# Performance work log

Measured on AMD Instinct MI355X. Metric: run time of the kernel, lower is better.

Reference implementation:

```python
import jax, jax.numpy as jnp
import numpy as np

N, H = 16, 200
EMB, H1, H2 = 64, 128, 64
NUM_SKILLS = 2000
D_USER, D_ITEM, D_LANG = 100, 100, 10
TIME_BINS = np.array([1, 3600, 24 * 3600, 7 * 24 * 3600], dtype=np.float32)
NUM_TIME_CATS = TIME_BINS.size + 2  # 6

# strictly-lower-triangular pair indices, row-major: pair (i, j) with j < i
PAIR_I, PAIR_J = np.tril_indices(H, k=-1)          # skill_indices, history_indices_selected
P = PAIR_I.size                                    # adjusted_history_len = H*(H-1)/2
ar = np.arange(H)
SUM_IDX = np.concatenate([ar * (ar - 1) // 2, [H * (H - 1) // 2]]).astype(np.int64)  # len H+1


def setup_inputs() -> dict:
    key = jax.random.key(0)
    ks = jax.random.split(key, 16)
    users = jax.random.normal(ks[0], (N, D_USER), jnp.float32)
    items = jax.random.normal(ks[1], (N * H, D_ITEM), jnp.float32)
    langs = jax.random.normal(ks[2], (N * H, D_LANG), jnp.float32)
    skills = jax.random.randint(ks[3], (N, H), 0, NUM_SKILLS)
    timestamps = jnp.sort(jax.random.uniform(ks[4], (N, H), jnp.float32) * 2e6, axis=1)
    targets = (jax.random.uniform(ks[5], (N, H)) > 0.5).astype(jnp.float32)
    mask = jnp.ones((N * H,), dtype=bool)
    emb_table = jax.random.normal(ks[6], (NUM_SKILLS, EMB), jnp.float32) * 0.1
    emb_table = emb_table.at[0].set(0.0)  # padding_idx=0
    W1 = jax.random.normal(ks[7], (H1, 2 * EMB + NUM_TIME_CATS), jnp.float32) * 0.05
    b1 = jnp.zeros((H1,), jnp.float32)
    W2 = jax.random.normal(ks[8], (H2, H1), jnp.float32) * 0.05
    b2 = jnp.zeros((H2,), jnp.float32)
    W3 = jax.random.normal(ks[9], (1, H2), jnp.float32) * 0.05
    b3 = jnp.zeros((1,), jnp.float32)
    num_features = D_USER + D_ITEM + D_LANG + NUM_SKILLS
    linW = jax.random.normal(ks[10], (1, num_features + 2 * NUM_SKILLS), jnp.float32) * 0.01
    linb = jnp.zeros((1,), jnp.float32)
    return {"users": users, "items": items, "langs": langs, "skills": skills,
            "timestamps": timestamps, "targets": targets, "mask": mask,
            "emb_table": emb_table, "W1": W1, "b1": b1, "W2": W2, "b2": b2,
            "W3": W3, "b3": b3, "linW": linW, "linb": linb}


def _forward(users, items, langs, skills, timestamps, targets, mask,
             emb_table, W1, b1, W2, b2, W3, b3, linW, linb):
    bins = jnp.asarray(TIME_BINS)
    pi = jnp.asarray(PAIR_I)
    pj = jnp.asarray(PAIR_J)
    # gather pair embeddings: [N*P, EMB]
    emb = emb_table[skills]                       # [N, H, EMB]
    e_i = emb[:, pi].reshape(-1, EMB)             # skill at position i
    e_j = emb[:, pj].reshape(-1, EMB)             # history skill j < i
    # time-delta categories
    dt = (timestamps[:, pi] - timestamps[:, pj]).reshape(-1)
    cats = jnp.sum(dt[:, None] > bins[None, :], axis=1) + 1
    pad = skills == 0
    pad_pair = pad[:, pi].reshape(-1) | pad[:, pj].reshape(-1)
    cats = jnp.where(pad_pair, 0, cats)
    dt_oh = jax.nn.one_hot(cats, NUM_TIME_CATS, dtype=jnp.float32)
    # pairwise similarity MLP -> tanh scalar, [N, P]
    x = jnp.concatenate([e_i, e_j, dt_oh], axis=1)
    h = jax.nn.relu(x @ W1.T + b1)
    h = jax.nn.relu(h @ W2.T + b2)
    sim = jnp.tanh(h @ W3.T + b3).reshape(N, P)

    sum_idx = jnp.asarray(SUM_IDX)

    def seg_sum(v):  # cumsum-based segment sum over pairs grouped by i -> [N, H]
        cs = jnp.concatenate([jnp.zeros((N, 1), v.dtype), jnp.cumsum(v, axis=1)], axis=1)
        return cs[:, sum_idx[1:]] - cs[:, sum_idx[:-1]]

    flat_skills = skills.reshape(-1)              # [N*H]
    padf = (flat_skills != 0).astype(jnp.float32)
    rows = jnp.arange(N * H)
    v_total = seg_sum(sim).reshape(-1) * padf
    v_correct = seg_sum(sim * targets[:, pi]).reshape(-1) * padf
    tcf = jnp.zeros((N * H, 2 * NUM_SKILLS), jnp.float32)
    tcf = tcf.at[rows, flat_skills].set(v_total)
    tcf = tcf.at[rows, flat_skills + NUM_SKILLS].set(v_correct)

    feats = jnp.concatenate([
        jnp.repeat(users, H, axis=0), items, langs,
        jax.nn.one_hot(flat_skills, NUM_SKILLS, dtype=jnp.float32), tcf], axis=1)
    logits = feats @ linW.T + linb                # [N*H, 1]
    preds = logits.reshape(-1)
    labels = targets.reshape(-1)
    maskf = mask.astype(jnp.float32)
    # BCEWithLogits (reduction='none') + z-term, z_weight=0.0; mask applied as weight
    bce = jnp.logaddexp(0.0, preds) - preds * labels
    eps = 1e-6
    yc = jnp.clip(labels, eps, 1.0 - eps)
    z = jnp.log(yc / (1.0 - yc))
    z_weight = 0.0
    loss = (bce + z_weight * jnp.square(z - preds)) * maskf
    return loss, jax.nn.sigmoid(preds), labels


def reference(users, items, langs, skills, timestamps, targets, mask,
              emb_table, W1, b1, W2, b2, W3, b3, linW, linb):
    return _forward(users, items, langs, skills, timestamps, targets, mask,
                    emb_table, W1, b1, W2, b2, W3, b3, linW, linb)
```

## Files before the change

### kernel.cpp

```cpp
#include <hip/hip_runtime.h>
#include <math.h>

#define N_B     16
#define H_LEN   200
#define NH      3200
#define EMB     64
#define HID1    128
#define HID2    64
#define NCAT    6
#define W1_COLS 134

#define TI 16
#define NTILE_I 13
#define NTRI (NTILE_I * (NTILE_I + 1) / 2)

#define WS_VT   0
#define WS_W2F  3200
#define WS_W1F  7296
#define WS_CF   15488

typedef __attribute__((ext_vector_type(8))) __bf16 bf16x8;
typedef __attribute__((ext_vector_type(8))) unsigned short ushort8;
typedef __attribute__((ext_vector_type(4))) float f32x4;

__device__ __forceinline__ unsigned short bfbits(float x) {
    return __builtin_bit_cast(unsigned short, (__bf16)x);
}

__global__ void k0_setup(const float* __restrict__ W1,
                         const float* __restrict__ b1,
                         const float* __restrict__ W2,
                         float* __restrict__ ws) {
    int idx = blockIdx.x * 256 + threadIdx.x;
    if (idx < 16384) {
        int e = idx & 7, l = (idx >> 3) & 63, ks = (idx >> 9) & 1;
        int nt = (idx >> 10) & 7, h = idx >> 13;
        int col = l & 15, quad = l >> 4;
        int c = nt * 16 + col;
        int kg = h * EMB + ks * 32 + quad * 8 + e;
        ((unsigned short*)(ws + WS_W1F))[idx] = bfbits(W1[c * W1_COLS + kg]);
        return;
    }
    idx -= 16384;
    if (idx < 8192) {
        int e = idx & 7, lane = (idx >> 3) & 63, f = idx >> 9;
        int mt = f >> 2, kk = f & 3, col = lane & 15, quad = lane >> 4;
        float w = W2[(mt * 16 + col) * HID1 + (kk * 4 + quad) * 8 + e];
        ((unsigned short*)(ws + WS_W2F))[idx] = bfbits(w);
        return;
    }
    idx -= 8192;
    if (idx < NCAT * HID1) {
        int c = idx >> 7, t = idx & 127;
        ws[WS_CF + idx] = W1[t * W1_COLS + 2 * EMB + c] + b1[t];
        return;
    }
    idx -= NCAT * HID1;
    if (idx < NH) ws[WS_VT + idx] = 0.f;
}

__global__ __launch_bounds__(256, 2)
void k2_mfma(const int* __restrict__ skills,
             const float* __restrict__ ts,
             const float* __restrict__ emb,
             const float* __restrict__ b2,
             const float* __restrict__ W3,
             const float* __restrict__ b3,
             float* __restrict__ ws) {
    __shared__ float esmI[TI][68];
    __shared__ float esmJ[TI][68];
    __shared__ float Asm[TI][132];
    __shared__ float Bsm[TI][132];
    __shared__ float Csm[NCAT][132];
    __shared__ float tsi[TI], tsj[TI];
    __shared__ int   ski[TI], skj[TI];

    int t = threadIdx.x, lane = t & 63, w = t >> 6;
    int col = lane & 15, quad = lane >> 4;

    int bid = blockIdx.x;
    int n = bid & 15;
    int tt = bid >> 4;
    int ti = (int)((sqrtf(8.f * (float)tt + 1.f) - 1.f) * 0.5f);
    while (ti * (ti + 1) / 2 > tt) --ti;
    while ((ti + 1) * (ti + 2) / 2 <= tt) ++ti;
    int tj = tt - ti * (ti + 1) / 2;
    int i0 = ti * TI, j0 = tj * TI;
    int base = n * H_LEN;
    bool diag = (ti == tj);

    {
        int r = t >> 4, c4 = t & 15;
        int gi = min(i0 + r, H_LEN - 1);
        int gj = min(j0 + r, H_LEN - 1);
        int si = skills[base + gi], sj2 = skills[base + gj];
        *(f32x4*)&esmI[r][c4 * 4] = *(const f32x4*)(emb + (size_t)si * EMB + c4 * 4);
        *(f32x4*)&esmJ[r][c4 * 4] = *(const f32x4*)(emb + (size_t)sj2 * EMB + c4 * 4);
        if (t < NCAT * 32) {
            int cr = t >> 5, cc = t & 31;
            *(f32x4*)&Csm[cr][cc * 4] = *(const f32x4*)(ws + WS_CF + cr * HID1 + cc * 4);
        }
        if (t < TI) {
            int gii = min(i0 + t, H_LEN - 1);
            int gjj = min(j0 + t, H_LEN - 1);
            tsi[t] = ts[base + gii]; ski[t] = skills[base + gii];
            tsj[t] = ts[base + gjj]; skj[t] = skills[base + gjj];
        }
    }
    __syncthreads();

    {
        int half = w >> 1;
        int ntb = (w & 1) * 4;
        const ushort8* w1f = (const ushort8*)(ws + WS_W1F) + half * 1024;
        float (*es)[68] = half ? esmJ : esmI;
        float (*zs)[132] = half ? Bsm : Asm;
        f32x4 acc[4] = {{0,0,0,0},{0,0,0,0},{0,0,0,0},{0,0,0,0}};
        #pragma unroll
        for (int ks = 0; ks < 2; ++ks) {
            f32x4 a0 = *(const f32x4*)&es[col][ks * 32 + quad * 8];
            f32x4 a1 = *(const f32x4*)&es[col][ks * 32 + quad * 8 + 4];
            bf16x8 af;
            #pragma unroll
            for (int e = 0; e < 4; ++e) { af[e] = (__bf16)a0[e]; af[4 + e] = (__bf16)a1[e]; }
            #pragma unroll
            for (int ntl = 0; ntl < 4; ++ntl) {
                bf16x8 bf = __builtin_bit_cast(bf16x8,
                    w1f[((ntb + ntl) * 2 + ks) * 64 + lane]);
                acc[ntl] = __builtin_amdgcn_mfma_f32_16x16x32_bf16(af, bf, acc[ntl], 0, 0, 0);
            }
        }
        #pragma unroll
        for (int ntl = 0; ntl < 4; ++ntl)
            #pragma unroll
            for (int r = 0; r < 4; ++r)
                zs[quad * 4 + r][(ntb + ntl) * 16 + col] = acc[ntl][r];
    }

    const ushort8* w2f = (const ushort8*)(ws + WS_W2F);
    bf16x8 afr[4][4];
    #pragma unroll
    for (int mt = 0; mt < 4; ++mt)
        #pragma unroll
        for (int kk = 0; kk < 4; ++kk)
            afr[mt][kk] = __builtin_bit_cast(bf16x8, w2f[(mt * 4 + kk) * 64 + lane]);
    f32x4 b2acc[4], w3f[4];
    #pragma unroll
    for (int mt = 0; mt < 4; ++mt)
        #pragma unroll
        for (int r = 0; r < 4; ++r) {
            int u = mt * 16 + quad * 4 + r;
            b2acc[mt][r] = b2[u];
            w3f[mt][r]   = W3[u];
        }
    float b3s = b3[0];
    __syncthreads();

    f32x4 braw[8];
    #pragma unroll
    for (int kk = 0; kk < 4; ++kk) {
        braw[2 * kk]     = *(const f32x4*)&Bsm[col][kk * 32 + quad * 8];
        braw[2 * kk + 1] = *(const f32x4*)&Bsm[col][kk * 32 + quad * 8 + 4];
    }
    int sj = skj[col]; float tsjv = tsj[col];

    #pragma unroll
    for (int s = 0; s < 4; ++s) {
        int ii = w * 4 + s;
        int gi = i0 + ii;
        if (gi >= H_LEN) continue;
        if (diag && ii == 0) continue;

        int si = ski[ii];  float tsiv = tsi[ii];
        float dtv = tsiv - tsjv;
        int cat = (si == 0 || sj == 0) ? 0
                : 1 + (dtv > 1.f) + (dtv > 3600.f) + (dtv > 86400.f) + (dtv > 604800.f);

        f32x4 acc[4];
        #pragma unroll
        for (int kk = 0; kk < 4; ++kk) {
            f32x4 a0 = *(const f32x4*)&Asm[ii][kk * 32 + quad * 8];
            f32x4 a1 = *(const f32x4*)&Asm[ii][kk * 32 + quad * 8 + 4];
            f32x4 c0 = *(const f32x4*)&Csm[cat][kk * 32 + quad * 8];
            f32x4 c1 = *(const f32x4*)&Csm[cat][kk * 32 + quad * 8 + 4];
            f32x4 t0 = a0 + braw[2 * kk] + c0;
            f32x4 t1 = a1 + braw[2 * kk + 1] + c1;
            t0 = __builtin_elementwise_max(t0, (f32x4)0.f);
            t1 = __builtin_elementwise_max(t1, (f32x4)0.f);
            bf16x8 v;
            #pragma unroll
            for (int e = 0; e < 4; ++e) { v[e] = (__bf16)t0[e]; v[4 + e] = (__bf16)t1[e]; }
            #pragma unroll
            for (int mt = 0; mt < 4; ++mt)
                acc[mt] = __builtin_amdgcn_mfma_f32_16x16x32_bf16(
                    afr[mt][kk], v, kk == 0 ? b2acc[mt] : acc[mt], 0, 0, 0);
        }

        f32x4 ps = {0.f, 0.f, 0.f, 0.f};
        #pragma unroll
        for (int mt = 0; mt < 4; ++mt) {
            f32x4 hp = __builtin_elementwise_max(acc[mt], (f32x4)0.f);
            ps = hp * w3f[mt] + ps;
        }
        float partial = (ps[0] + ps[1]) + (ps[2] + ps[3]);
        partial += __shfl_xor(partial, 16);
        partial += __shfl_xor(partial, 32);
        float xc = fminf(fmaxf(partial + b3s, -15.f), 15.f);
        float e2 = __expf(2.f * xc);
        float sim = (e2 - 1.f) / (e2 + 1.f);

        int gj = j0 + col;
        bool valid = (gj < gi);
        sim = valid ? sim : 0.f;
        sim += __shfl_xor(sim, 1);
        sim += __shfl_xor(sim, 2);
        sim += __shfl_xor(sim, 4);
        sim += __shfl_xor(sim, 8);
        if (lane == 0) atomicAdd(&ws[WS_VT + base + gi], sim);
    }
}

__global__ __launch_bounds__(256)
void k3_final(const float* __restrict__ users,
              const float* __restrict__ items,
              const float* __restrict__ langs,
              const int* __restrict__ skills,
              const float* __restrict__ targets,
              const float* __restrict__ linW,
              const float* __restrict__ linb,
              const float* __restrict__ ws,
              float* __restrict__ out) {
    int r = blockIdx.x * 4 + (threadIdx.x >> 6);
    int lane = threadIdx.x & 63;
    int n = r / H_LEN;
    float acc = 0.f;
    for (int idx = lane; idx < 210; idx += 64) {
        float f;
        if (idx < 100)      f = users[n * 100 + idx];
        else if (idx < 200) f = items[r * 100 + (idx - 100)];
        else                f = langs[r * 10 + (idx - 200)];
        acc = fmaf(f, linW[idx], acc);
    }
    #pragma unroll
    for (int off = 32; off > 0; off >>= 1) acc += __shfl_xor(acc, off);
    if (lane == 0) {
        int s = skills[r];
        float tgt = targets[r];
        float vtv = ws[WS_VT + r];
        if (s == 0) vtv = 0.f;
        float vcv = vtv * tgt;
        float logit = acc + linW[210 + s] + vtv * linW[2210 + s]
                    + vcv * linW[4210 + s] + linb[0];
        float sp = logit > 0.f ? logit + log1pf(expf(-logit)) : log1pf(expf(logit));
        float loss = sp - logit * tgt;
        float sig = 1.f / (1.f + expf(-logit));
        out[r]          = loss;
        out[NH + r]     = sig;
        out[2 * NH + r] = tgt;
    }
}

extern "C" void kernel_launch(void* const* d_in, const int* in_sizes, int n_in,
                              void* d_out, int out_size, void* d_ws, size_t ws_size,
                              hipStream_t stream) {
    const float* users   = (const float*)d_in[0];
    const float* items   = (const float*)d_in[1];
    const float* langs   = (const float*)d_in[2];
    const int*   skills  = (const int*)d_in[3];
    const float* ts      = (const float*)d_in[4];
    const float* targets = (const float*)d_in[5];
    const float* emb     = (const float*)d_in[7];
    const float* W1      = (const float*)d_in[8];
    const float* b1      = (const float*)d_in[9];
    const float* W2      = (const float*)d_in[10];
    const float* b2      = (const float*)d_in[11];
    const float* W3      = (const float*)d_in[12];
    const float* b3      = (const float*)d_in[13];
    const float* linW    = (const float*)d_in[14];
    const float* linb    = (const float*)d_in[15];
    float* ws  = (float*)d_ws;
    float* out = (float*)d_out;

    hipLaunchKernelGGL(k0_setup, dim3(112), dim3(256), 0, stream, W1, b1, W2, ws);
    hipLaunchKernelGGL(k2_mfma, dim3(N_B * NTRI), dim3(256), 0, stream,
                       skills, ts, emb, b2, W3, b3, ws);
    hipLaunchKernelGGL(k3_final, dim3(NH / 4), dim3(256), 0, stream,
                       users, items, langs, skills, targets, linW, linb, ws, out);
}
```

Measured before the change: 111.4 us.

## Drop setup kernel, convert weights inline, and replace atomics with per-tile partial sums

Removes the separate weight-preparation kernel. The MFMA kernel now reads W1, W2 and b1 directly in fp32 and converts them to bf16 in registers. The atomicAdd accumulation, and the zeroing it needed, is replaced by each tile writing its partial similarity into a per-row, per-tile slot, which the final kernel sums with a wavefront shuffle reduction. This saves a kernel launch and the atomic contention. In exchange, every block repeats the weight conversion and does strided fp32 global loads instead of reading pre-swizzled bf16 fragments.

```diff
diff --git a/kernel.cpp b/kernel.cpp
--- a/kernel.cpp
+++ b/kernel.cpp
@@ -15,54 +15,18 @@
 #define NTRI (NTILE_I * (NTILE_I + 1) / 2)
 
 #define WS_VT   0
-#define WS_W2F  3200
-#define WS_W1F  7296
-#define WS_CF   15488
 
 typedef __attribute__((ext_vector_type(8))) __bf16 bf16x8;
-typedef __attribute__((ext_vector_type(8))) unsigned short ushort8;
 typedef __attribute__((ext_vector_type(4))) float f32x4;
-
-__device__ __forceinline__ unsigned short bfbits(float x) {
-    return __builtin_bit_cast(unsigned short, (__bf16)x);
-}
-
-__global__ void k0_setup(const float* __restrict__ W1,
-                         const float* __restrict__ b1,
-                         const float* __restrict__ W2,
-                         float* __restrict__ ws) {
-    int idx = blockIdx.x * 256 + threadIdx.x;
-    if (idx < 16384) {
-        int e = idx & 7, l = (idx >> 3) & 63, ks = (idx >> 9) & 1;
-        int nt = (idx >> 10) & 7, h = idx >> 13;
-        int col = l & 15, quad = l >> 4;
-        int c = nt * 16 + col;
-        int kg = h * EMB + ks * 32 + quad * 8 + e;
-        ((unsigned short*)(ws + WS_W1F))[idx] = bfbits(W1[c * W1_COLS + kg]);
-        return;
-    }
-    idx -= 16384;
-    if (idx < 8192) {
-        int e = idx & 7, lane = (idx >> 3) & 63, f = idx >> 9;
-        int mt = f >> 2, kk = f & 3, col = lane & 15, quad = lane >> 4;
-        float w = W2[(mt * 16 + col) * HID1 + (kk * 4 + quad) * 8 + e];
-        ((unsigned short*)(ws + WS_W2F))[idx] = bfbits(w);
-        return;
-    }
-    idx -= 8192;
-    if (idx < NCAT * HID1) {
-        int c = idx >> 7, t = idx & 127;
-        ws[WS_CF + idx] = W1[t * W1_COLS + 2 * EMB + c] + b1[t];
-        return;
-    }
-    idx -= NCAT * HID1;
-    if (idx < NH) ws[WS_VT + idx] = 0.f;
-}
+typedef __attribute__((ext_vector_type(2))) float f32x2;
 
 __global__ __launch_bounds__(256, 2)
 void k2_mfma(const int* __restrict__ skills,
              const float* __restrict__ ts,
              const float* __restrict__ emb,
+             const float* __restrict__ W1,
+             const float* __restrict__ b1,
+             const float* __restrict__ W2,
              const float* __restrict__ b2,
              const float* __restrict__ W3,
              const float* __restrict__ b3,
@@ -98,7 +62,11 @@
         *(f32x4*)&esmJ[r][c4 * 4] = *(const f32x4*)(emb + (size_t)sj2 * EMB + c4 * 4);
         if (t < NCAT * 32) {
             int cr = t >> 5, cc = t & 31;
-            *(f32x4*)&Csm[cr][cc * 4] = *(const f32x4*)(ws + WS_CF + cr * HID1 + cc * 4);
+            #pragma unroll
+            for (int e = 0; e < 4; ++e) {
+                int u = cc * 4 + e;
+                Csm[cr][u] = W1[(size_t)u * W1_COLS + 2 * EMB + cr] + b1[u];
+            }
         }
         if (t < TI) {
             int gii = min(i0 + t, H_LEN - 1);
@@ -112,7 +80,6 @@
     {
         int half = w >> 1;
         int ntb = (w & 1) * 4;
-        const ushort8* w1f = (const ushort8*)(ws + WS_W1F) + half * 1024;
         float (*es)[68] = half ? esmJ : esmI;
         float (*zs)[132] = half ? Bsm : Asm;
         f32x4 acc[4] = {{0,0,0,0},{0,0,0,0},{0,0,0,0},{0,0,0,0}};
@@ -125,8 +92,17 @@
             for (int e = 0; e < 4; ++e) { af[e] = (__bf16)a0[e]; af[4 + e] = (__bf16)a1[e]; }
             #pragma unroll
             for (int ntl = 0; ntl < 4; ++ntl) {
-                bf16x8 bf = __builtin_bit_cast(bf16x8,
-                    w1f[((ntb + ntl) * 2 + ks) * 64 + lane]);
+                const float* wp = W1 + (size_t)((ntb + ntl) * 16 + col) * W1_COLS
+                                  + half * 64 + ks * 32 + quad * 8;
+                f32x2 p0 = *(const f32x2*)wp;
+                f32x2 p1 = *(const f32x2*)(wp + 2);
+                f32x2 p2 = *(const f32x2*)(wp + 4);
+                f32x2 p3 = *(const f32x2*)(wp + 6);
+                bf16x8 bf;
+                bf[0] = (__bf16)p0[0]; bf[1] = (__bf16)p0[1];
+                bf[2] = (__bf16)p1[0]; bf[3] = (__bf16)p1[1];
+                bf[4] = (__bf16)p2[0]; bf[5] = (__bf16)p2[1];
+                bf[6] = (__bf16)p3[0]; bf[7] = (__bf16)p3[1];
                 acc[ntl] = __builtin_amdgcn_mfma_f32_16x16x32_bf16(af, bf, acc[ntl], 0, 0, 0);
             }
         }
@@ -137,13 +113,19 @@
                 zs[quad * 4 + r][(ntb + ntl) * 16 + col] = acc[ntl][r];
     }
 
-    const ushort8* w2f = (const ushort8*)(ws + WS_W2F);
     bf16x8 afr[4][4];
     #pragma unroll
     for (int mt = 0; mt < 4; ++mt)
         #pragma unroll
-        for (int kk = 0; kk < 4; ++kk)
-            afr[mt][kk] = __builtin_bit_cast(bf16x8, w2f[(mt * 4 + kk) * 64 + lane]);
+        for (int kk = 0; kk < 4; ++kk) {
+            const float* wp = W2 + (size_t)(mt * 16 + col) * HID1 + (kk * 4 + quad) * 8;
+            f32x4 w0 = *(const f32x4*)wp;
+            f32x4 w1v = *(const f32x4*)(wp + 4);
+            bf16x8 v;
+            #pragma unroll
+            for (int e = 0; e < 4; ++e) { v[e] = (__bf16)w0[e]; v[4 + e] = (__bf16)w1v[e]; }
+            afr[mt][kk] = v;
+        }
     f32x4 b2acc[4], w3f[4];
     #pragma unroll
     for (int mt = 0; mt < 4; ++mt)
@@ -216,7 +198,7 @@
         sim += __shfl_xor(sim, 2);
         sim += __shfl_xor(sim, 4);
         sim += __shfl_xor(sim, 8);
-        if (lane == 0) atomicAdd(&ws[WS_VT + base + gi], sim);
+        if (lane == 0) ws[WS_VT + (size_t)(base + gi) * 16 + tj] = sim;
     }
 }
 
@@ -233,6 +215,7 @@
     int r = blockIdx.x * 4 + (threadIdx.x >> 6);
     int lane = threadIdx.x & 63;
     int n = r / H_LEN;
+    int gi = r - n * H_LEN;
     float acc = 0.f;
     for (int idx = lane; idx < 210; idx += 64) {
         float f;
@@ -243,10 +226,18 @@
     }
     #pragma unroll
     for (int off = 32; off > 0; off >>= 1) acc += __shfl_xor(acc, off);
+
+    int cnt = (gi >> 4) + ((gi & 15) ? 1 : 0);
+    float v = (lane < cnt) ? ws[WS_VT + (size_t)r * 16 + lane] : 0.f;
+    v += __shfl_xor(v, 1);
+    v += __shfl_xor(v, 2);
+    v += __shfl_xor(v, 4);
+    v += __shfl_xor(v, 8);
+
     if (lane == 0) {
         int s = skills[r];
         float tgt = targets[r];
-        float vtv = ws[WS_VT + r];
+        float vtv = v;
         if (s == 0) vtv = 0.f;
         float vcv = vtv * tgt;
         float logit = acc + linW[210 + s] + vtv * linW[2210 + s]
@@ -281,9 +272,8 @@
     float* ws  = (float*)d_ws;
     float* out = (float*)d_out;
 
-    hipLaunchKernelGGL(k0_setup, dim3(112), dim3(256), 0, stream, W1, b1, W2, ws);
     hipLaunchKernelGGL(k2_mfma, dim3(N_B * NTRI), dim3(256), 0, stream,
-                       skills, ts, emb, b2, W3, b3, ws);
+                       skills, ts, emb, W1, b1, W2, b2, W3, b3, ws);
     hipLaunchKernelGGL(k3_final, dim3(NH / 4), dim3(256), 0, stream,
                        users, items, langs, skills, targets, linW, linb, ws, out);
 }
```

Result: slower. 126.0 us (+13.2%).

## Make k2 blocks persistent over tile pairs with prefetch and per-tile partial sums

Applied to the files above, without the earlier changes.

Each k2 block now handles seven consecutive triangular tile pairs with 512 threads, keeping W1 fragments in registers across iterations. It prefetches the next tile's embeddings and timestamps while the current tile computes. Atomic accumulation into the per-row sum is replaced by writing per-(row, j-tile) partials, which k3 reduces with lane shuffles, so k0 no longer needs to zero the workspace. The cost is fewer blocks (208 instead of 1456), which may underfill the device, plus extra barriers per iteration.

```diff
diff --git a/kernel.cpp b/kernel.cpp
--- a/kernel.cpp
+++ b/kernel.cpp
@@ -13,11 +13,13 @@
 #define TI 16
 #define NTILE_I 13
 #define NTRI (NTILE_I * (NTILE_I + 1) / 2)
+#define PAIRS_PER_BLK 7
+#define NSLICE 13
 
 #define WS_VT   0
-#define WS_W2F  3200
-#define WS_W1F  7296
-#define WS_CF   15488
+#define WS_W2F  51200
+#define WS_W1F  55296
+#define WS_CF   63488
 
 typedef __attribute__((ext_vector_type(8))) __bf16 bf16x8;
 typedef __attribute__((ext_vector_type(8))) unsigned short ushort8;
@@ -51,15 +53,12 @@
     }
     idx -= 8192;
     if (idx < NCAT * HID1) {
-        int c = idx >> 7, t = idx & 127;
-        ws[WS_CF + idx] = W1[t * W1_COLS + 2 * EMB + c] + b1[t];
-        return;
-    }
-    idx -= NCAT * HID1;
-    if (idx < NH) ws[WS_VT + idx] = 0.f;
-}
-
-__global__ __launch_bounds__(256, 2)
+        int c = idx >> 7, u = idx & 127;
+        ws[WS_CF + idx] = W1[u * W1_COLS + 2 * EMB + c] + b1[u];
+    }
+}
+
+__global__ __launch_bounds__(512, 2)
 void k2_mfma(const int* __restrict__ skills,
              const float* __restrict__ ts,
              const float* __restrict__ emb,
@@ -72,71 +71,35 @@
     __shared__ float Asm[TI][132];
     __shared__ float Bsm[TI][132];
     __shared__ float Csm[NCAT][132];
-    __shared__ float tsi[TI], tsj[TI];
-    __shared__ int   ski[TI], skj[TI];
+    __shared__ float tsiS[TI], tsjS[TI];
+    __shared__ int   skiS[TI], skjS[TI];
 
     int t = threadIdx.x, lane = t & 63, w = t >> 6;
     int col = lane & 15, quad = lane >> 4;
 
     int bid = blockIdx.x;
     int n = bid & 15;
-    int tt = bid >> 4;
+    int s = bid >> 4;
+    int base = n * H_LEN;
+    int tt = s * PAIRS_PER_BLK;
     int ti = (int)((sqrtf(8.f * (float)tt + 1.f) - 1.f) * 0.5f);
     while (ti * (ti + 1) / 2 > tt) --ti;
     while ((ti + 1) * (ti + 2) / 2 <= tt) ++ti;
     int tj = tt - ti * (ti + 1) / 2;
-    int i0 = ti * TI, j0 = tj * TI;
-    int base = n * H_LEN;
-    bool diag = (ti == tj);
-
-    {
-        int r = t >> 4, c4 = t & 15;
-        int gi = min(i0 + r, H_LEN - 1);
-        int gj = min(j0 + r, H_LEN - 1);
-        int si = skills[base + gi], sj2 = skills[base + gj];
-        *(f32x4*)&esmI[r][c4 * 4] = *(const f32x4*)(emb + (size_t)si * EMB + c4 * 4);
-        *(f32x4*)&esmJ[r][c4 * 4] = *(const f32x4*)(emb + (size_t)sj2 * EMB + c4 * 4);
-        if (t < NCAT * 32) {
-            int cr = t >> 5, cc = t & 31;
-            *(f32x4*)&Csm[cr][cc * 4] = *(const f32x4*)(ws + WS_CF + cr * HID1 + cc * 4);
-        }
-        if (t < TI) {
-            int gii = min(i0 + t, H_LEN - 1);
-            int gjj = min(j0 + t, H_LEN - 1);
-            tsi[t] = ts[base + gii]; ski[t] = skills[base + gii];
-            tsj[t] = ts[base + gjj]; skj[t] = skills[base + gjj];
-        }
-    }
-    __syncthreads();
-
-    {
-        int half = w >> 1;
-        int ntb = (w & 1) * 4;
-        const ushort8* w1f = (const ushort8*)(ws + WS_W1F) + half * 1024;
-        float (*es)[68] = half ? esmJ : esmI;
-        float (*zs)[132] = half ? Bsm : Asm;
-        f32x4 acc[4] = {{0,0,0,0},{0,0,0,0},{0,0,0,0},{0,0,0,0}};
-        #pragma unroll
-        for (int ks = 0; ks < 2; ++ks) {
-            f32x4 a0 = *(const f32x4*)&es[col][ks * 32 + quad * 8];
-            f32x4 a1 = *(const f32x4*)&es[col][ks * 32 + quad * 8 + 4];
-            bf16x8 af;
-            #pragma unroll
-            for (int e = 0; e < 4; ++e) { af[e] = (__bf16)a0[e]; af[4 + e] = (__bf16)a1[e]; }
-            #pragma unroll
-            for (int ntl = 0; ntl < 4; ++ntl) {
-                bf16x8 bf = __builtin_bit_cast(bf16x8,
-                    w1f[((ntb + ntl) * 2 + ks) * 64 + lane]);
-                acc[ntl] = __builtin_amdgcn_mfma_f32_16x16x32_bf16(af, bf, acc[ntl], 0, 0, 0);
-            }
-        }
-        #pragma unroll
-        for (int ntl = 0; ntl < 4; ++ntl)
-            #pragma unroll
-            for (int r = 0; r < 4; ++r)
-                zs[quad * 4 + r][(ntb + ntl) * 16 + col] = acc[ntl][r];
-    }
-
+
+    if (t < 192) {
+        int cr = t >> 5, cc = t & 31;
+        *(f32x4*)&Csm[cr][cc * 4] = *(const f32x4*)(ws + WS_CF + cr * HID1 + cc * 4);
+    }
+    int half = w >> 2, ntq = (w & 3) * 2;
+    const ushort8* w1f = (const ushort8*)(ws + WS_W1F);
+    bf16x8 w1frag[2][2];
+    #pragma unroll
+    for (int l = 0; l < 2; ++l)
+        #pragma unroll
+        for (int ks = 0; ks < 2; ++ks)
+            w1frag[l][ks] = __builtin_bit_cast(bf16x8,
+                w1f[((half * 8 + ntq + l) * 2 + ks) * 64 + lane]);
     const ushort8* w2f = (const ushort8*)(ws + WS_W2F);
     bf16x8 afr[4][4];
     #pragma unroll
@@ -144,79 +107,155 @@
         #pragma unroll
         for (int kk = 0; kk < 4; ++kk)
             afr[mt][kk] = __builtin_bit_cast(bf16x8, w2f[(mt * 4 + kk) * 64 + lane]);
-    f32x4 b2acc[4], w3f[4];
+    f32x4 b2acc[4], w3f4[4];
     #pragma unroll
     for (int mt = 0; mt < 4; ++mt)
         #pragma unroll
         for (int r = 0; r < 4; ++r) {
             int u = mt * 16 + quad * 4 + r;
             b2acc[mt][r] = b2[u];
-            w3f[mt][r]   = W3[u];
+            w3f4[mt][r]  = W3[u];
         }
     float b3s = b3[0];
+
+    int side = t >> 8, rr = (t >> 4) & 15, c4 = t & 15;
+    {
+        int g = min((side ? tj : ti) * TI + rr, H_LEN - 1);
+        int sk = skills[base + g];
+        f32x4 v = *(const f32x4*)(emb + (size_t)sk * EMB + c4 * 4);
+        if (side) *(f32x4*)&esmJ[rr][c4 * 4] = v;
+        else      *(f32x4*)&esmI[rr][c4 * 4] = v;
+    }
+    if (t < 32) {
+        int sd = t >> 4, r2 = t & 15;
+        int g = min((sd ? tj : ti) * TI + r2, H_LEN - 1);
+        float tv = ts[base + g]; int sv = skills[base + g];
+        if (sd) { tsjS[r2] = tv; skjS[r2] = sv; }
+        else    { tsiS[r2] = tv; skiS[r2] = sv; }
+    }
     __syncthreads();
 
-    f32x4 braw[8];
-    #pragma unroll
-    for (int kk = 0; kk < 4; ++kk) {
-        braw[2 * kk]     = *(const f32x4*)&Bsm[col][kk * 32 + quad * 8];
-        braw[2 * kk + 1] = *(const f32x4*)&Bsm[col][kk * 32 + quad * 8 + 4];
-    }
-    int sj = skj[col]; float tsjv = tsj[col];
-
-    #pragma unroll
-    for (int s = 0; s < 4; ++s) {
-        int ii = w * 4 + s;
-        int gi = i0 + ii;
-        if (gi >= H_LEN) continue;
-        if (diag && ii == 0) continue;
-
-        int si = ski[ii];  float tsiv = tsi[ii];
-        float dtv = tsiv - tsjv;
-        int cat = (si == 0 || sj == 0) ? 0
-                : 1 + (dtv > 1.f) + (dtv > 3600.f) + (dtv > 86400.f) + (dtv > 604800.f);
-
-        f32x4 acc[4];
+    for (int it = 0; it < PAIRS_PER_BLK; ++it) {
+        bool diag = (ti == tj);
+        int i0 = ti * TI, j0 = tj * TI;
+
+        {
+            float (*es)[68]  = half ? esmJ : esmI;
+            float (*zs)[132] = half ? Bsm : Asm;
+            f32x4 acc0 = {0.f,0.f,0.f,0.f}, acc1 = {0.f,0.f,0.f,0.f};
+            #pragma unroll
+            for (int ks = 0; ks < 2; ++ks) {
+                f32x4 a0 = *(const f32x4*)&es[col][ks * 32 + quad * 8];
+                f32x4 a1 = *(const f32x4*)&es[col][ks * 32 + quad * 8 + 4];
+                bf16x8 af;
+                #pragma unroll
+                for (int e = 0; e < 4; ++e) { af[e] = (__bf16)a0[e]; af[4 + e] = (__bf16)a1[e]; }
+                acc0 = __builtin_amdgcn_mfma_f32_16x16x32_bf16(af, w1frag[0][ks], acc0, 0, 0, 0);
+                acc1 = __builtin_amdgcn_mfma_f32_16x16x32_bf16(af, w1frag[1][ks], acc1, 0, 0, 0);
+            }
+            #pragma unroll
+            for (int r = 0; r < 4; ++r) {
+                zs[quad * 4 + r][(ntq + 0) * 16 + col] = acc0[r];
+                zs[quad * 4 + r][(ntq + 1) * 16 + col] = acc1[r];
+            }
+        }
+
+        int nti = ti, ntj = tj + 1;
+        if (ntj > nti) { ++nti; ntj = 0; }
+        bool hasNext = (it + 1 < PAIRS_PER_BLK);
+        f32x4 pref = {0.f,0.f,0.f,0.f};
+        float ptv = 0.f; int psv = 0;
+        if (hasNext) {
+            int g = min((side ? ntj : nti) * TI + rr, H_LEN - 1);
+            int sk = skills[base + g];
+            pref = *(const f32x4*)(emb + (size_t)sk * EMB + c4 * 4);
+            if (t < 32) {
+                int sd = t >> 4, r2 = t & 15;
+                int g2 = min((sd ? ntj : nti) * TI + r2, H_LEN - 1);
+                ptv = ts[base + g2]; psv = skills[base + g2];
+            }
+        }
+        int sj = skjS[col]; float tsjv = tsjS[col];
+        int   siA[2]; float tsiA[2];
+        #pragma unroll
+        for (int ss = 0; ss < 2; ++ss) { siA[ss] = skiS[w * 2 + ss]; tsiA[ss] = tsiS[w * 2 + ss]; }
+
+        __syncthreads();
+
+        if (hasNext) {
+            if (side) *(f32x4*)&esmJ[rr][c4 * 4] = pref;
+            else      *(f32x4*)&esmI[rr][c4 * 4] = pref;
+            if (t < 32) {
+                int sd = t >> 4, r2 = t & 15;
+                if (sd) { tsjS[r2] = ptv; skjS[r2] = psv; }
+                else    { tsiS[r2] = ptv; skiS[r2] = psv; }
+            }
+        }
+
+        f32x4 braw[8];
         #pragma unroll
         for (int kk = 0; kk < 4; ++kk) {
-            f32x4 a0 = *(const f32x4*)&Asm[ii][kk * 32 + quad * 8];
-            f32x4 a1 = *(const f32x4*)&Asm[ii][kk * 32 + quad * 8 + 4];
-            f32x4 c0 = *(const f32x4*)&Csm[cat][kk * 32 + quad * 8];
-            f32x4 c1 = *(const f32x4*)&Csm[cat][kk * 32 + quad * 8 + 4];
-            f32x4 t0 = a0 + braw[2 * kk] + c0;
-            f32x4 t1 = a1 + braw[2 * kk + 1] + c1;
-            t0 = __builtin_elementwise_max(t0, (f32x4)0.f);
-            t1 = __builtin_elementwise_max(t1, (f32x4)0.f);
-            bf16x8 v;
+            braw[2 * kk]     = *(const f32x4*)&Bsm[col][kk * 32 + quad * 8];
+            braw[2 * kk + 1] = *(const f32x4*)&Bsm[col][kk * 32 + quad * 8 + 4];
+        }
+
+        #pragma unroll
+        for (int ss = 0; ss < 2; ++ss) {
+            int ii = w * 2 + ss;
+            int gi = i0 + ii;
+            if (gi >= H_LEN) continue;
+            if (diag && ii == 0) continue;
+
+            int si = siA[ss]; float tsiv = tsiA[ss];
+            float dtv = tsiv - tsjv;
+            int cat = (si == 0 || sj == 0) ? 0
+                    : 1 + (dtv > 1.f) + (dtv > 3600.f) + (dtv > 86400.f) + (dtv > 604800.f);
+
+            f32x4 acc[4];
             #pragma unroll
-            for (int e = 0; e < 4; ++e) { v[e] = (__bf16)t0[e]; v[4 + e] = (__bf16)t1[e]; }
+            for (int kk = 0; kk < 4; ++kk) {
+                f32x4 a0 = *(const f32x4*)&Asm[ii][kk * 32 + quad * 8];
+                f32x4 a1 = *(const f32x4*)&Asm[ii][kk * 32 + quad * 8 + 4];
+                f32x4 c0 = *(const f32x4*)&Csm[cat][kk * 32 + quad * 8];
+                f32x4 c1 = *(const f32x4*)&Csm[cat][kk * 32 + quad * 8 + 4];
+                f32x4 t0 = a0 + braw[2 * kk] + c0;
+                f32x4 t1 = a1 + braw[2 * kk + 1] + c1;
+                t0 = __builtin_elementwise_max(t0, (f32x4)0.f);
+                t1 = __builtin_elementwise_max(t1, (f32x4)0.f);
+                bf16x8 v;
+                #pragma unroll
+                for (int e = 0; e < 4; ++e) { v[e] = (__bf16)t0[e]; v[4 + e] = (__bf16)t1[e]; }
+                #pragma unroll
+                for (int mt = 0; mt < 4; ++mt)
+                    acc[mt] = __builtin_amdgcn_mfma_f32_16x16x32_bf16(
+                        afr[mt][kk], v, kk == 0 ? b2acc[mt] : acc[mt], 0, 0, 0);
+            }
+
+            f32x4 ps = {0.f, 0.f, 0.f, 0.f};
             #pragma unroll
-            for (int mt = 0; mt < 4; ++mt)
-                acc[mt] = __builtin_amdgcn_mfma_f32_16x16x32_bf16(
-                    afr[mt][kk], v, kk == 0 ? b2acc[mt] : acc[mt], 0, 0, 0);
-        }
-
-        f32x4 ps = {0.f, 0.f, 0.f, 0.f};
-        #pragma unroll
-        for (int mt = 0; mt < 4; ++mt) {
-            f32x4 hp = __builtin_elementwise_max(acc[mt], (f32x4)0.f);
-            ps = hp * w3f[mt] + ps;
-        }
-        float partial = (ps[0] + ps[1]) + (ps[2] + ps[3]);
-        partial += __shfl_xor(partial, 16);
-        partial += __shfl_xor(partial, 32);
-        float xc = fminf(fmaxf(partial + b3s, -15.f), 15.f);
-        float e2 = __expf(2.f * xc);
-        float sim = (e2 - 1.f) / (e2 + 1.f);
-
-        int gj = j0 + col;
-        bool valid = (gj < gi);
-        sim = valid ? sim : 0.f;
-        sim += __shfl_xor(sim, 1);
-        sim += __shfl_xor(sim, 2);
-        sim += __shfl_xor(sim, 4);
-        sim += __shfl_xor(sim, 8);
-        if (lane == 0) atomicAdd(&ws[WS_VT + base + gi], sim);
+            for (int mt = 0; mt < 4; ++mt) {
+                f32x4 hp = __builtin_elementwise_max(acc[mt], (f32x4)0.f);
+                ps = hp * w3f4[mt] + ps;
+            }
+            float partial = (ps[0] + ps[1]) + (ps[2] + ps[3]);
+            partial += __shfl_xor(partial, 16);
+            partial += __shfl_xor(partial, 32);
+            float xc = fminf(fmaxf(partial + b3s, -15.f), 15.f);
+            float e2 = __expf(2.f * xc);
+            float sim = (e2 - 1.f) / (e2 + 1.f);
+
+            int gj = j0 + col;
+            bool valid = (gj < gi);
+            sim = valid ? sim : 0.f;
+            sim += __shfl_xor(sim, 1);
+            sim += __shfl_xor(sim, 2);
+            sim += __shfl_xor(sim, 4);
+            sim += __shfl_xor(sim, 8);
+            if (lane == 0) ws[WS_VT + (size_t)(base + gi) * 16 + tj] = sim;
+        }
+
+        __syncthreads();
+        ti = nti; tj = ntj;
     }
 }
 
@@ -233,6 +272,7 @@
     int r = blockIdx.x * 4 + (threadIdx.x >> 6);
     int lane = threadIdx.x & 63;
     int n = r / H_LEN;
+    int gi = r - n * H_LEN;
     float acc = 0.f;
     for (int idx = lane; idx < 210; idx += 64) {
         float f;
@@ -243,10 +283,18 @@
     }
     #pragma unroll
     for (int off = 32; off > 0; off >>= 1) acc += __shfl_xor(acc, off);
+
+    int cnt = (gi >> 4) + ((gi & 15) ? 1 : 0);
+    float v = (lane < cnt) ? ws[WS_VT + (size_t)r * 16 + lane] : 0.f;
+    v += __shfl_xor(v, 1);
+    v += __shfl_xor(v, 2);
+    v += __shfl_xor(v, 4);
+    v += __shfl_xor(v, 8);
+
     if (lane == 0) {
         int s = skills[r];
         float tgt = targets[r];
-        float vtv = ws[WS_VT + r];
+        float vtv = v;
         if (s == 0) vtv = 0.f;
         float vcv = vtv * tgt;
         float logit = acc + linW[210 + s] + vtv * linW[2210 + s]
@@ -281,8 +329,8 @@
     float* ws  = (float*)d_ws;
     float* out = (float*)d_out;
 
-    hipLaunchKernelGGL(k0_setup, dim3(112), dim3(256), 0, stream, W1, b1, W2, ws);
-    hipLaunchKernelGGL(k2_mfma, dim3(N_B * NTRI), dim3(256), 0, stream,
+    hipLaunchKernelGGL(k0_setup, dim3(99), dim3(256), 0, stream, W1, b1, W2, ws);
+    hipLaunchKernelGGL(k2_mfma, dim3(N_B * NSLICE), dim3(512), 0, stream,
                        skills, ts, emb, b2, W3, b3, ws);
     hipLaunchKernelGGL(k3_final, dim3(NH / 4), dim3(256), 0, stream,
                        users, items, langs, skills, targets, linW, linb, ws, out);
```

After: 114.2 us. +2.6%, slower.
